# Optimization experiments

Hardware: AMD Instinct MI355X
Metric: run time of the kernel (lower is better)

## Reference

```python
import jax, jax.numpy as jnp
import numpy as np

HIDDEN = 1024
NUM_HEADS = 16
HEAD_DIM = HIDDEN // NUM_HEADS  # 64
MLP_HIDDEN = 4096
RMS_EPS = 1e-6


def setup_inputs() -> dict:
    key = jax.random.key(0)
    ks = jax.random.split(key, 4)
    B, L = 2, 2048
    x = jax.random.normal(ks[0], (B, L, HIDDEN), dtype=jnp.float32)
    pe = jax.random.normal(ks[1], (1, 1, L, HEAD_DIM // 2, 2, 2), dtype=jnp.float32)
    W1 = jax.random.normal(ks[2], (HIDDEN, 3 * HIDDEN + MLP_HIDDEN), dtype=jnp.float32) * (HIDDEN ** -0.5)
    b1 = jnp.zeros((3 * HIDDEN + MLP_HIDDEN,), dtype=jnp.float32)
    W2 = jax.random.normal(ks[3], (HIDDEN + MLP_HIDDEN, HIDDEN), dtype=jnp.float32) * ((HIDDEN + MLP_HIDDEN) ** -0.5)
    b2 = jnp.zeros((HIDDEN,), dtype=jnp.float32)
    q_scale = jnp.ones((HEAD_DIM,), dtype=jnp.float32)
    k_scale = jnp.ones((HEAD_DIM,), dtype=jnp.float32)
    return {"x": x, "pe": pe, "W1": W1, "b1": b1, "W2": W2, "b2": b2,
            "q_scale": q_scale, "k_scale": k_scale}


def _rms_norm(t, scale):
    # RMSNorm over last dim (head_dim) with learnable scale (flux QKNorm)
    rrms = jax.lax.rsqrt(jnp.mean(jnp.square(t), axis=-1, keepdims=True) + RMS_EPS)
    return t * rrms * scale


def _apply_rope(xq, xk, pe):
    # pe: [1,1,L,D/2,2,2]; x*: [B,H,L,D]
    def rope(t):
        t_ = t.reshape(*t.shape[:-1], -1, 1, 2)  # [B,H,L,D/2,1,2]
        out = pe[..., 0] * t_[..., 0] + pe[..., 1] * t_[..., 1]  # [B,H,L,D/2,2]
        return out.reshape(*t.shape)
    return rope(xq), rope(xk)


def reference(x, pe, W1, b1, W2, b2, q_scale, k_scale):
    B, L, _ = x.shape
    h = x @ W1 + b1  # [B,L,3H+Mh]
    qkv, mlp = h[..., : 3 * HIDDEN], h[..., 3 * HIDDEN:]
    # 'B L (K H D) -> K B H L D'
    qkv = qkv.reshape(B, L, 3, NUM_HEADS, HEAD_DIM).transpose(2, 0, 3, 1, 4)
    q, k, v = qkv[0], qkv[1], qkv[2]
    q = _rms_norm(q, q_scale)
    k = _rms_norm(k, k_scale)
    q, k = _apply_rope(q, k, pe)
    scale = HEAD_DIM ** -0.5
    scores = jnp.einsum('bhqd,bhkd->bhqk', q, k) * scale
    attn = jnp.einsum('bhqk,bhkd->bhqd', jax.nn.softmax(scores, axis=-1), v)
    attn = attn.transpose(0, 2, 1, 3).reshape(B, L, HIDDEN)  # 'B H L D -> B L (H D)'
    out = jnp.concatenate((attn, jax.nn.gelu(mlp)), axis=2) @ W2 + b2
    return out
```

## Files before the change

### kernel.cpp

```cpp
#include <hip/hip_runtime.h>

typedef __bf16 bf16;
typedef __bf16 bf16x8 __attribute__((ext_vector_type(8)));
typedef float f32x4 __attribute__((ext_vector_type(4)));
typedef float f32x16 __attribute__((ext_vector_type(16)));

#define GLDS16(gp, lp) __builtin_amdgcn_global_load_lds( \
    (__attribute__((address_space(1))) void*)(gp), \
    (__attribute__((address_space(3))) void*)(lp), 16, 0, 0)

__device__ inline float ex2(float x) { return exp2f(x); }


__global__ void f2b_kernel(const float* __restrict__ src, bf16* __restrict__ dst, long n) {
    long i = ((long)blockIdx.x * 256 + threadIdx.x) * 4;
    if (i + 3 < n) {
        float4 v = *(const float4*)&src[i];
        dst[i + 0] = (bf16)v.x;
        dst[i + 1] = (bf16)v.y;
        dst[i + 2] = (bf16)v.z;
        dst[i + 3] = (bf16)v.w;
    }
}

__global__ __launch_bounds__(256) void transpose_f2b(const float* __restrict__ W,
                                                     bf16* __restrict__ WT,
                                                     int K, int N) {
    __shared__ float tile[32][33];
    int tx = threadIdx.x & 31;
    int ty = threadIdx.x >> 5;
    int n0 = blockIdx.x * 32;
    int k0 = blockIdx.y * 32;
#pragma unroll
    for (int i = 0; i < 4; ++i)
        tile[ty + i * 8][tx] = W[(long)(k0 + ty + i * 8) * N + n0 + tx];
    __syncthreads();
#pragma unroll
    for (int i = 0; i < 4; ++i)
        WT[(long)(n0 + ty + i * 8) * K + k0 + tx] = (bf16)tile[tx][ty + i * 8];
}

template <bool OUT_F32>
__global__ __launch_bounds__(256) void gemm_bt(const bf16* __restrict__ A,
                                               const bf16* __restrict__ BT,
                                               const float* __restrict__ bias,
                                               void* __restrict__ C,
                                               int M, int N, int K) {
    __shared__ bf16 Asm[128 * 32];
    __shared__ bf16 Bsm[128 * 32];
    int tid = threadIdx.x;
    int w = tid >> 6, l = tid & 63;
    int wr = w >> 1, wc = w & 1;
    int bm = blockIdx.x * 128;
    int bn = blockIdx.y * 128;

    f32x4 acc[4][4] = {};

    int arow = l >> 2;
    int acol = (l & 3) * 8;
    int fr = l & 15;
    int fk = (l >> 4) * 8;

    int nk = K >> 5;
    for (int kt = 0; kt < nk; ++kt) {
        int k0 = kt * 32;
#pragma unroll
        for (int it = 0; it < 2; ++it) {
            int c = it * 4 + w;
            const bf16* ga = A + (long)(bm + c * 16 + arow) * K + k0 + acol;
            GLDS16(ga, &Asm[c * 512]);
            const bf16* gb = BT + (long)(bn + c * 16 + arow) * K + k0 + acol;
            GLDS16(gb, &Bsm[c * 512]);
        }
        asm volatile("s_waitcnt vmcnt(0)" ::: "memory");
        __syncthreads();

        bf16x8 af[4], bfr[4];
#pragma unroll
        for (int m = 0; m < 4; ++m)
            af[m] = *(const bf16x8*)&Asm[(wr * 64 + m * 16 + fr) * 32 + fk];
#pragma unroll
        for (int n = 0; n < 4; ++n)
            bfr[n] = *(const bf16x8*)&Bsm[(wc * 64 + n * 16 + fr) * 32 + fk];
#pragma unroll
        for (int m = 0; m < 4; ++m)
#pragma unroll
            for (int n = 0; n < 4; ++n)
                acc[m][n] = __builtin_amdgcn_mfma_f32_16x16x32_bf16(af[m], bfr[n], acc[m][n], 0, 0, 0);
        __syncthreads();
    }

    int orow0 = bm + wr * 64;
    int ocol0 = bn + wc * 64;
#pragma unroll
    for (int m = 0; m < 4; ++m) {
        int row = orow0 + m * 16 + (l >> 4) * 4;
#pragma unroll
        for (int n = 0; n < 4; ++n) {
            int col = ocol0 + n * 16 + (l & 15);
            float bv = bias[col];
#pragma unroll
            for (int r = 0; r < 4; ++r) {
                float v = acc[m][n][r] + bv;
                if (OUT_F32)
                    ((float*)C)[(long)(row + r) * N + col] = v;
                else
                    ((bf16*)C)[(long)(row + r) * N + col] = (bf16)v;
            }
        }
    }
}

__global__ __launch_bounds__(256) void gemm_bt_splitk(const bf16* __restrict__ A,
                                                      const bf16* __restrict__ BT,
                                                      float* __restrict__ part,
                                                      int M, int N, int K, int kchunk) {
    __shared__ bf16 Asm[128 * 32];
    __shared__ bf16 Bsm[128 * 32];
    int tid = threadIdx.x;
    int w = tid >> 6, l = tid & 63;
    int wr = w >> 1, wc = w & 1;
    int bm = blockIdx.x * 128;
    int bn = blockIdx.y * 128;
    int kz = blockIdx.z;

    f32x4 acc[4][4] = {};

    int arow = l >> 2;
    int acol = (l & 3) * 8;
    int fr = l & 15;
    int fk = (l >> 4) * 8;

    int nk = kchunk >> 5;
    for (int kt = 0; kt < nk; ++kt) {
        int k0 = kz * kchunk + kt * 32;
#pragma unroll
        for (int it = 0; it < 2; ++it) {
            int c = it * 4 + w;
            const bf16* ga = A + (long)(bm + c * 16 + arow) * K + k0 + acol;
            GLDS16(ga, &Asm[c * 512]);
            const bf16* gb = BT + (long)(bn + c * 16 + arow) * K + k0 + acol;
            GLDS16(gb, &Bsm[c * 512]);
        }
        asm volatile("s_waitcnt vmcnt(0)" ::: "memory");
        __syncthreads();

        bf16x8 af[4], bfr[4];
#pragma unroll
        for (int m = 0; m < 4; ++m)
            af[m] = *(const bf16x8*)&Asm[(wr * 64 + m * 16 + fr) * 32 + fk];
#pragma unroll
        for (int n = 0; n < 4; ++n)
            bfr[n] = *(const bf16x8*)&Bsm[(wc * 64 + n * 16 + fr) * 32 + fk];
#pragma unroll
        for (int m = 0; m < 4; ++m)
#pragma unroll
            for (int n = 0; n < 4; ++n)
                acc[m][n] = __builtin_amdgcn_mfma_f32_16x16x32_bf16(af[m], bfr[n], acc[m][n], 0, 0, 0);
        __syncthreads();
    }

    float* cz = part + (long)kz * M * N;
    int orow0 = bm + wr * 64;
    int ocol0 = bn + wc * 64;
#pragma unroll
    for (int m = 0; m < 4; ++m) {
        int row = orow0 + m * 16 + (l >> 4) * 4;
#pragma unroll
        for (int n = 0; n < 4; ++n) {
            int col = ocol0 + n * 16 + (l & 15);
#pragma unroll
            for (int r = 0; r < 4; ++r)
                cz[(long)(row + r) * N + col] = acc[m][n][r];
        }
    }
}

__global__ __launch_bounds__(256) void reduce4_kernel(const float* __restrict__ part,
                                                      const float* __restrict__ b2,
                                                      float* __restrict__ out) {
    const long stride4 = 4096L * 1024 / 4;
#pragma unroll
    for (int it = 0; it < 2; ++it) {
        long i4 = (long)blockIdx.x * 512 + it * 256 + threadIdx.x;
        float4 s = *(const float4*)&b2[(i4 * 4) & 1023];
        const float4* p = (const float4*)part;
#pragma unroll
        for (int z = 0; z < 4; ++z) {
            float4 v = p[z * stride4 + i4];
            s.x += v.x; s.y += v.y; s.z += v.z; s.w += v.w;
        }
        *(float4*)&out[i4 * 4] = s;
    }
}

__global__ __launch_bounds__(256) void qkv_kernel(const bf16* __restrict__ h,
                                                  const float* __restrict__ pe,
                                                  const float* __restrict__ qsc_,
                                                  const float* __restrict__ ksc_,
                                                  bf16* __restrict__ qo,
                                                  bf16* __restrict__ ko) {
    int t = blockIdx.x;
    int b = t >> 11;
    int lpos = t & 2047;
    int wv = threadIdx.x >> 6;
    int d = threadIdx.x & 63;
    const bf16* hrow = h + (long)t * 7168;
    float pe0 = pe[lpos * 128 + (d >> 1) * 4 + (d & 1) * 2 + 0];
    float pe1 = pe[lpos * 128 + (d >> 1) * 4 + (d & 1) * 2 + 1];
    float qsc = qsc_[d], ksc = ksc_[d];
#pragma unroll 1
    for (int it = 0; it < 4; ++it) {
        int hh = wv * 4 + it;
        float qv = (float)hrow[hh * 64 + d];
        float kv = (float)hrow[1024 + hh * 64 + d];
        float ssq = qv * qv, ssk = kv * kv;
#pragma unroll
        for (int off = 1; off < 64; off <<= 1) {
            ssq += __shfl_xor(ssq, off, 64);
            ssk += __shfl_xor(ssk, off, 64);
        }
        float qn = qv * rsqrtf(ssq * (1.0f / 64.0f) + 1e-6f) * qsc;
        float kn = kv * rsqrtf(ssk * (1.0f / 64.0f) + 1e-6f) * ksc;
        float qe = __shfl(qn, d & 62, 64), qodd = __shfl(qn, d | 1, 64);
        float ke = __shfl(kn, d & 62, 64), kodd = __shfl(kn, d | 1, 64);
        float qr = (pe0 * qe + pe1 * qodd) * 0.18033688011112042f;
        float kr = pe0 * ke + pe1 * kodd;
        long base = ((long)(b * 16 + hh) * 2048 + lpos) * 64 + d;
        qo[base] = (bf16)qr;
        ko[base] = (bf16)kr;
    }
}

__global__ __launch_bounds__(256) void vtrans_kernel(const bf16* __restrict__ h,
                                                     bf16* __restrict__ vT) {
    __shared__ unsigned short tile[64 * 65];
    int bh = blockIdx.x;
    int b = bh >> 4, hh = bh & 15;
    int l0 = blockIdx.y * 64;
    int tid = threadIdx.x;

    int r = tid >> 3, c = tid & 7;
#pragma unroll
    for (int p = 0; p < 2; ++p) {
        int row = r + p * 32;
        const bf16* src = h + (long)(b * 2048 + l0 + row) * 7168 + 2048 + hh * 64 + c * 8;
        bf16x8 v = *(const bf16x8*)src;
        union { bf16x8 v; unsigned short s[8]; } u; u.v = v;
#pragma unroll
        for (int e = 0; e < 8; ++e) tile[row * 65 + c * 8 + e] = u.s[e];
    }
    __syncthreads();

#pragma unroll
    for (int p = 0; p < 2; ++p) {
        int idx = tid + p * 256;
        int d = idx >> 3, kg = idx & 7;
        union { bf16x8 v; unsigned short s[8]; } u;
#pragma unroll
        for (int e = 0; e < 8; ++e) u.s[e] = tile[(kg * 8 + e) * 65 + d];
        *(bf16x8*)&vT[((long)bh * 64 + d) * 2048 + l0 + kg * 8] = u.v;
    }
}

__global__ void gelu_kernel(const bf16* __restrict__ h, bf16* __restrict__ cat) {
    long e = ((long)blockIdx.x * 256 + threadIdx.x) * 8;
    int t = (int)(e >> 12);
    int j = (int)(e & 4095);
    bf16x8 v = *(const bf16x8*)&h[(long)t * 7168 + 3072 + j];
    bf16x8 o;
#pragma unroll
    for (int r = 0; r < 8; ++r) {
        float x = (float)v[r];
        float g = 0.5f * x * (1.0f + tanhf(0.7978845608028654f * (x + 0.044715f * x * x * x)));
        o[r] = (bf16)g;
    }
    *(bf16x8*)&cat[(long)t * 5120 + 1024 + j] = o;
}

__global__ __launch_bounds__(512) void attn_kernel(const bf16* __restrict__ qg,
                                                   const bf16* __restrict__ kg_,
                                                   const bf16* __restrict__ vT,
                                                   bf16* __restrict__ cat) {
    __shared__ __align__(16) char lds[65536];
    char* Kl0 = lds;
    char* Kl1 = lds + 8192;
    char* Vl0 = lds + 16384;
    char* Vl1 = lds + 24576;

    int bidx = blockIdx.x;
    int bh = bidx & 31;
    int qblk = bidx >> 5;
    int b = bh >> 4, hh = bh & 15;
    int tid = threadIdx.x;
    int wv = tid >> 6, l = tid & 63;
    int h = l >> 5, ln = l & 31;
    int sw = (ln & 7) << 4;

    char* Pw = lds + 32768 + wv * 4096;

    const bf16* qbase = qg + ((long)bh * 2048 + qblk * 256 + wv * 32 + ln) * 64 + h * 8;
    bf16x8 qf[4];
#pragma unroll
    for (int ds = 0; ds < 4; ++ds) qf[ds] = *(const bf16x8*)(qbase + ds * 16);

    f32x16 Oa0 = {}, Oa1 = {};
    float m = -1e30f, lsum = 0.0f;

    int kr = tid >> 3, kg = tid & 7;
    int swb = (kg * 16) ^ ((kr & 7) << 4);
    const bf16* gK = kg_ + ((long)bh * 2048 + kr) * 64 + kg * 8;
    const bf16* gV = vT + ((long)bh * 64 + kr) * 2048 + kg * 8;

    bf16x8 rk = *(const bf16x8*)gK;
    bf16x8 rv = *(const bf16x8*)gV;
    *(bf16x8*)(Kl0 + kr * 128 + swb) = rk;
    *(bf16x8*)(Vl0 + kr * 128 + swb) = rv;
    __syncthreads();

    int c = 0;
    for (int t = 0; t < 32; ++t) {
        if (t < 31) {
            rk = *(const bf16x8*)(gK + (long)(t + 1) * 4096);
            rv = *(const bf16x8*)(gV + (t + 1) * 64);
        }
        const char* Kc = c ? Kl1 : Kl0;
        const char* Vc = c ? Vl1 : Vl0;

        f32x16 S0 = {}, S1 = {};
#pragma unroll
        for (int ds = 0; ds < 4; ++ds) {
            bf16x8 kf0 = *(const bf16x8*)(Kc + ln * 128 + ((ds * 32 + h * 16) ^ sw));
            bf16x8 kf1 = *(const bf16x8*)(Kc + (32 + ln) * 128 + ((ds * 32 + h * 16) ^ sw));
            S0 = __builtin_amdgcn_mfma_f32_32x32x16_bf16(kf0, qf[ds], S0, 0, 0, 0);
            S1 = __builtin_amdgcn_mfma_f32_32x32x16_bf16(kf1, qf[ds], S1, 0, 0, 0);
        }

        float tmax = S0[0];
#pragma unroll
        for (int r = 1; r < 16; ++r) tmax = fmaxf(tmax, S0[r]);
#pragma unroll
        for (int r = 0; r < 16; ++r) tmax = fmaxf(tmax, S1[r]);
        tmax = fmaxf(tmax, __shfl_xor(tmax, 32, 64));

        if (!__all(tmax - m <= 8.0f)) {
            float mn = fmaxf(m, tmax);
            float es = ex2(m - mn);
            lsum *= es;
            m = mn;
#pragma unroll
            for (int r = 0; r < 16; ++r) {
                int rowq = (r & 3) + 8 * (r >> 2) + 4 * h;
                float esr = __shfl(es, rowq, 64);
                Oa0[r] *= esr;
                Oa1[r] *= esr;
            }
        }

        float ps = 0.0f;
#pragma unroll
        for (int kvt = 0; kvt < 2; ++kvt) {
            float p[16];
#pragma unroll
            for (int r = 0; r < 16; ++r) {
                float v = ex2((kvt ? S1[r] : S0[r]) - m);
                p[r] = v;
                ps += v;
            }
#pragma unroll
            for (int i = 0; i < 8; ++i) {
                union { bf16 bb[2]; unsigned u; } pr;
                pr.bb[0] = (bf16)p[2 * i];
                pr.bb[1] = (bf16)p[2 * i + 1];
                int kv = ((2 * i) & 3) + 8 * (i >> 1) + 4 * h + 32 * kvt;
                *(unsigned*)(Pw + ln * 128 + ((kv * 2) ^ sw)) = pr.u;
            }
        }
        lsum += ps + __shfl_xor(ps, 32, 64);

        asm volatile("s_waitcnt lgkmcnt(0)" ::: "memory");

        bf16x8 pa[4];
#pragma unroll
        for (int s = 0; s < 4; ++s)
            pa[s] = *(const bf16x8*)(Pw + ln * 128 + ((s * 32 + h * 16) ^ sw));

#pragma unroll
        for (int s = 0; s < 4; ++s) {
            bf16x8 vf0 = *(const bf16x8*)(Vc + ln * 128 + ((s * 32 + h * 16) ^ sw));
            bf16x8 vf1 = *(const bf16x8*)(Vc + (32 + ln) * 128 + ((s * 32 + h * 16) ^ sw));
            Oa0 = __builtin_amdgcn_mfma_f32_32x32x16_bf16(pa[s], vf0, Oa0, 0, 0, 0);
            Oa1 = __builtin_amdgcn_mfma_f32_32x32x16_bf16(pa[s], vf1, Oa1, 0, 0, 0);
        }

        __syncthreads();
        if (t < 31) {
            char* Kn = c ? Kl0 : Kl1;
            char* Vn = c ? Vl0 : Vl1;
            *(bf16x8*)(Kn + kr * 128 + swb) = rk;
            *(bf16x8*)(Vn + kr * 128 + swb) = rv;
        }
        __syncthreads();
        c ^= 1;
    }

#pragma unroll
    for (int r = 0; r < 16; ++r) {
        int rowq = (r & 3) + 8 * (r >> 2) + 4 * h;
        float ls = __shfl(lsum, rowq, 64);
        float inv = 1.0f / ls;
        long trow = (long)b * 2048 + qblk * 256 + wv * 32 + rowq;
        cat[trow * 5120 + hh * 64 + ln] = (bf16)(Oa0[r] * inv);
        cat[trow * 5120 + hh * 64 + 32 + ln] = (bf16)(Oa1[r] * inv);
    }
}


extern "C" void kernel_launch(void* const* d_in, const int* in_sizes, int n_in,
                              void* d_out, int out_size, void* d_ws, size_t ws_size,
                              hipStream_t stream) {
    const float* x  = (const float*)d_in[0];
    const float* pe = (const float*)d_in[1];
    const float* W1 = (const float*)d_in[2];
    const float* b1 = (const float*)d_in[3];
    const float* W2 = (const float*)d_in[4];
    const float* b2 = (const float*)d_in[5];
    const float* qs = (const float*)d_in[6];
    const float* ks = (const float*)d_in[7];
    float* out = (float*)d_out;

    char* ws = (char*)d_ws;
    bf16* xb  = (bf16*)(ws);
    bf16* w1t = (bf16*)(ws + 8388608);
    bf16* w2t = (bf16*)(ws + 23068672);
    bf16* h   = (bf16*)(ws + 33554432);
    bf16* qb  = (bf16*)(ws + 92274688);
    bf16* kb  = (bf16*)(ws + 100663296);
    bf16* vT  = (bf16*)(ws + 109051904);
    bf16* cat = (bf16*)(ws + 117440512);
    float* part = (float*)(ws + 33554432);

    f2b_kernel<<<4096, 256, 0, stream>>>(x, xb, 4194304L);
    transpose_f2b<<<dim3(224, 32), 256, 0, stream>>>(W1, w1t, 1024, 7168);
    transpose_f2b<<<dim3(32, 160), 256, 0, stream>>>(W2, w2t, 5120, 1024);

    gemm_bt<false><<<dim3(32, 56), 256, 0, stream>>>(xb, w1t, b1, h, 4096, 7168, 1024);

    qkv_kernel<<<4096, 256, 0, stream>>>(h, pe, qs, ks, qb, kb);
    vtrans_kernel<<<dim3(32, 32), 256, 0, stream>>>(h, vT);
    gelu_kernel<<<8192, 256, 0, stream>>>(h, cat);

    attn_kernel<<<256, 512, 0, stream>>>(qb, kb, vT, cat);

    gemm_bt_splitk<<<dim3(32, 8, 4), 256, 0, stream>>>(cat, w2t, part, 4096, 1024, 5120, 1280);
    reduce4_kernel<<<2048, 256, 0, stream>>>(part, b2, out);
}
```

Baseline: 298.3 us.

## Replace GEMMs with pipelined 256x256 tile kernel and fuse GELU into epilogue

Both GEMMs now use one templated kernel with 512 threads and 256x256 output tiles. It double-buffers LDS with asynchronous global-to-LDS loads, staggers the A and B prefetches, raises wave priority around the MFMA bursts, and swizzles the block order for the first GEMM. The first GEMM's epilogue applies GELU to the MLP columns and writes them straight into the concatenated buffer, so the separate GELU kernel and its extra pass over memory are gone. The larger tiles raise register and LDS pressure, and the fewer blocks may leave some CUs idle for the second GEMM.

```diff
diff --git a/kernel.cpp b/kernel.cpp
--- a/kernel.cpp
+++ b/kernel.cpp
@@ -8,6 +8,10 @@
 #define GLDS16(gp, lp) __builtin_amdgcn_global_load_lds( \
     (__attribute__((address_space(1))) void*)(gp), \
     (__attribute__((address_space(3))) void*)(lp), 16, 0, 0)
+
+#define BARRIER() asm volatile("s_barrier" ::: "memory")
+#define LGKM0_FENCE() do { asm volatile("s_waitcnt lgkmcnt(0)" ::: "memory"); \
+                           __builtin_amdgcn_sched_barrier(0); } while (0)
 
 __device__ inline float ex2(float x) { return exp2f(x); }
 
@@ -40,138 +44,140 @@
         WT[(long)(n0 + ty + i * 8) * K + k0 + tx] = (bf16)tile[tx][ty + i * 8];
 }
 
-template <bool OUT_F32>
-__global__ __launch_bounds__(256) void gemm_bt(const bf16* __restrict__ A,
-                                               const bf16* __restrict__ BT,
-                                               const float* __restrict__ bias,
-                                               void* __restrict__ C,
-                                               int M, int N, int K) {
-    __shared__ bf16 Asm[128 * 32];
-    __shared__ bf16 Bsm[128 * 32];
+template <int EPI>
+__global__ __launch_bounds__(512, 2) void gemm256(const bf16* __restrict__ A_,
+                                                  const bf16* __restrict__ BT_,
+                                                  const float* __restrict__ bias,
+                                                  void* __restrict__ C0,
+                                                  void* __restrict__ C1,
+                                                  int M, int N, int K, int kch) {
+    __shared__ __align__(16) char ldsb[65536];
+
+    int bx, by, k0base = 0;
+    if (EPI == 0) {
+        int bid = blockIdx.x;
+        int swz = (bid & 7) * 56 + (bid >> 3);
+        bx = swz & 15; by = swz >> 4;
+    } else {
+        bx = blockIdx.x; by = blockIdx.y;
+        k0base = blockIdx.z * kch;
+    }
+    int bm = bx * 256, bn = by * 256;
+    int NT = kch >> 5;
+
     int tid = threadIdx.x;
     int w = tid >> 6, l = tid & 63;
-    int wr = w >> 1, wc = w & 1;
-    int bm = blockIdx.x * 128;
-    int bn = blockIdx.y * 128;
-
-    f32x4 acc[4][4] = {};
-
-    int arow = l >> 2;
-    int acol = (l & 3) * 8;
-    int fr = l & 15;
-    int fk = (l >> 4) * 8;
-
-    int nk = K >> 5;
-    for (int kt = 0; kt < nk; ++kt) {
-        int k0 = kt * 32;
-#pragma unroll
-        for (int it = 0; it < 2; ++it) {
-            int c = it * 4 + w;
-            const bf16* ga = A + (long)(bm + c * 16 + arow) * K + k0 + acol;
-            GLDS16(ga, &Asm[c * 512]);
-            const bf16* gb = BT + (long)(bn + c * 16 + arow) * K + k0 + acol;
-            GLDS16(gb, &Bsm[c * 512]);
-        }
-        asm volatile("s_waitcnt vmcnt(0)" ::: "memory");
-        __syncthreads();
+    int wr = w >> 2, wc = w & 3;
+    int fr = l & 15, g = l >> 4;
+
+    int srow = tid >> 2;
+    int scol = (tid & 3) * 8;
+    const bf16* gA = A_ + (long)(bm + srow) * K + k0base + scol;
+    const bf16* gB = BT_ + (long)(bn + srow) * K + k0base + scol;
+
+    int abase = (wr * 128 + fr) * 64 + g * 16;
+    int bbase = (wc * 64 + fr) * 64 + g * 16;
+
+    f32x4 acc[8][4] = {};
+
+    GLDS16(gA, ldsb + tid * 16);
+    GLDS16(gA + (long)128 * K, ldsb + 8192 + tid * 16);
+    GLDS16(gB, ldsb + 16384 + tid * 16);
+    GLDS16(gB + (long)128 * K, ldsb + 16384 + 8192 + tid * 16);
+    GLDS16(gB + 32, ldsb + 32768 + 16384 + tid * 16);
+    GLDS16(gB + 32 + (long)128 * K, ldsb + 32768 + 16384 + 8192 + tid * 16);
+    asm volatile("s_waitcnt vmcnt(2)" ::: "memory");
+    BARRIER();
+
+    for (int u = 0; u < NT; ++u) {
+        const char* Ab = ldsb + (u & 1) * 32768;
+        const char* Bb = Ab + 16384;
+        int nxt = (~u) & 1;
 
         bf16x8 af[4], bfr[4];
 #pragma unroll
-        for (int m = 0; m < 4; ++m)
-            af[m] = *(const bf16x8*)&Asm[(wr * 64 + m * 16 + fr) * 32 + fk];
+        for (int i = 0; i < 4; ++i)
+            af[i] = *(const bf16x8*)(Ab + abase + i * 1024);
 #pragma unroll
         for (int n = 0; n < 4; ++n)
-            bfr[n] = *(const bf16x8*)&Bsm[(wc * 64 + n * 16 + fr) * 32 + fk];
-#pragma unroll
-        for (int m = 0; m < 4; ++m)
-#pragma unroll
-            for (int n = 0; n < 4; ++n)
-                acc[m][n] = __builtin_amdgcn_mfma_f32_16x16x32_bf16(af[m], bfr[n], acc[m][n], 0, 0, 0);
-        __syncthreads();
-    }
-
-    int orow0 = bm + wr * 64;
-    int ocol0 = bn + wc * 64;
-#pragma unroll
-    for (int m = 0; m < 4; ++m) {
-        int row = orow0 + m * 16 + (l >> 4) * 4;
-#pragma unroll
-        for (int n = 0; n < 4; ++n) {
-            int col = ocol0 + n * 16 + (l & 15);
-            float bv = bias[col];
-#pragma unroll
-            for (int r = 0; r < 4; ++r) {
-                float v = acc[m][n][r] + bv;
-                if (OUT_F32)
-                    ((float*)C)[(long)(row + r) * N + col] = v;
-                else
-                    ((bf16*)C)[(long)(row + r) * N + col] = (bf16)v;
+            bfr[n] = *(const bf16x8*)(Bb + bbase + n * 1024);
+        if (u + 1 < NT) {
+            const bf16* s = gA + (u + 1) * 32;
+            GLDS16(s, ldsb + nxt * 32768 + tid * 16);
+            GLDS16(s + (long)128 * K, ldsb + nxt * 32768 + 8192 + tid * 16);
+        }
+        BARRIER();
+        LGKM0_FENCE();
+        __builtin_amdgcn_s_setprio(1);
+#pragma unroll
+        for (int n = 0; n < 4; ++n)
+#pragma unroll
+            for (int i = 0; i < 4; ++i)
+                acc[i][n] = __builtin_amdgcn_mfma_f32_16x16x32_bf16(af[i], bfr[n], acc[i][n], 0, 0, 0);
+        __builtin_amdgcn_s_setprio(0);
+        BARRIER();
+
+#pragma unroll
+        for (int i = 0; i < 4; ++i)
+            af[i] = *(const bf16x8*)(Ab + abase + (4 + i) * 1024);
+        if (u + 2 < NT) {
+            const bf16* s = gB + (u + 2) * 32;
+            GLDS16(s, ldsb + (u & 1) * 32768 + 16384 + tid * 16);
+            GLDS16(s + (long)128 * K, ldsb + (u & 1) * 32768 + 16384 + 8192 + tid * 16);
+        }
+        BARRIER();
+        LGKM0_FENCE();
+        __builtin_amdgcn_s_setprio(1);
+#pragma unroll
+        for (int n = 0; n < 4; ++n)
+#pragma unroll
+            for (int i = 0; i < 4; ++i)
+                acc[4 + i][n] = __builtin_amdgcn_mfma_f32_16x16x32_bf16(af[i], bfr[n], acc[4 + i][n], 0, 0, 0);
+        __builtin_amdgcn_s_setprio(0);
+        if (u < NT - 2) {
+            asm volatile("s_waitcnt vmcnt(2)" ::: "memory");
+        } else {
+            asm volatile("s_waitcnt vmcnt(0)" ::: "memory");
+        }
+        BARRIER();
+    }
+
+    int r4 = (l >> 4) * 4;
+    if (EPI == 0) {
+        bf16* hp = (bf16*)C0;
+        bf16* cat = (bf16*)C1;
+        bool gel = (bn >= 3072);
+#pragma unroll
+        for (int mi = 0; mi < 8; ++mi) {
+            int row = bm + wr * 128 + mi * 16 + r4;
+#pragma unroll
+            for (int n = 0; n < 4; ++n) {
+                int col = bn + wc * 64 + n * 16 + fr;
+                float bv = bias[col];
+#pragma unroll
+                for (int r = 0; r < 4; ++r) {
+                    float v = acc[mi][n][r] + bv;
+                    if (gel) {
+                        float gg = 0.5f * v * (1.0f + tanhf(0.7978845608028654f * (v + 0.044715f * v * v * v)));
+                        cat[(long)(row + r) * 5120 + 1024 + col - 3072] = (bf16)gg;
+                    } else {
+                        hp[(long)(row + r) * N + col] = (bf16)v;
+                    }
+                }
             }
         }
-    }
-}
-
-__global__ __launch_bounds__(256) void gemm_bt_splitk(const bf16* __restrict__ A,
-                                                      const bf16* __restrict__ BT,
-                                                      float* __restrict__ part,
-                                                      int M, int N, int K, int kchunk) {
-    __shared__ bf16 Asm[128 * 32];
-    __shared__ bf16 Bsm[128 * 32];
-    int tid = threadIdx.x;
-    int w = tid >> 6, l = tid & 63;
-    int wr = w >> 1, wc = w & 1;
-    int bm = blockIdx.x * 128;
-    int bn = blockIdx.y * 128;
-    int kz = blockIdx.z;
-
-    f32x4 acc[4][4] = {};
-
-    int arow = l >> 2;
-    int acol = (l & 3) * 8;
-    int fr = l & 15;
-    int fk = (l >> 4) * 8;
-
-    int nk = kchunk >> 5;
-    for (int kt = 0; kt < nk; ++kt) {
-        int k0 = kz * kchunk + kt * 32;
-#pragma unroll
-        for (int it = 0; it < 2; ++it) {
-            int c = it * 4 + w;
-            const bf16* ga = A + (long)(bm + c * 16 + arow) * K + k0 + acol;
-            GLDS16(ga, &Asm[c * 512]);
-            const bf16* gb = BT + (long)(bn + c * 16 + arow) * K + k0 + acol;
-            GLDS16(gb, &Bsm[c * 512]);
-        }
-        asm volatile("s_waitcnt vmcnt(0)" ::: "memory");
-        __syncthreads();
-
-        bf16x8 af[4], bfr[4];
-#pragma unroll
-        for (int m = 0; m < 4; ++m)
-            af[m] = *(const bf16x8*)&Asm[(wr * 64 + m * 16 + fr) * 32 + fk];
-#pragma unroll
-        for (int n = 0; n < 4; ++n)
-            bfr[n] = *(const bf16x8*)&Bsm[(wc * 64 + n * 16 + fr) * 32 + fk];
-#pragma unroll
-        for (int m = 0; m < 4; ++m)
-#pragma unroll
-            for (int n = 0; n < 4; ++n)
-                acc[m][n] = __builtin_amdgcn_mfma_f32_16x16x32_bf16(af[m], bfr[n], acc[m][n], 0, 0, 0);
-        __syncthreads();
-    }
-
-    float* cz = part + (long)kz * M * N;
-    int orow0 = bm + wr * 64;
-    int ocol0 = bn + wc * 64;
-#pragma unroll
-    for (int m = 0; m < 4; ++m) {
-        int row = orow0 + m * 16 + (l >> 4) * 4;
-#pragma unroll
-        for (int n = 0; n < 4; ++n) {
-            int col = ocol0 + n * 16 + (l & 15);
-#pragma unroll
-            for (int r = 0; r < 4; ++r)
-                cz[(long)(row + r) * N + col] = acc[m][n][r];
+    } else {
+        float* cz = (float*)C0 + (long)blockIdx.z * M * N;
+#pragma unroll
+        for (int mi = 0; mi < 8; ++mi) {
+            int row = bm + wr * 128 + mi * 16 + r4;
+#pragma unroll
+            for (int n = 0; n < 4; ++n) {
+                int col = bn + wc * 64 + n * 16 + fr;
+#pragma unroll
+                for (int r = 0; r < 4; ++r)
+                    cz[(long)(row + r) * N + col] = acc[mi][n][r];
+            }
         }
     }
 }
@@ -251,7 +257,6 @@
         for (int e = 0; e < 8; ++e) tile[row * 65 + c * 8 + e] = u.s[e];
     }
     __syncthreads();
-
 #pragma unroll
     for (int p = 0; p < 2; ++p) {
         int idx = tid + p * 256;
@@ -261,21 +266,6 @@
         for (int e = 0; e < 8; ++e) u.s[e] = tile[(kg * 8 + e) * 65 + d];
         *(bf16x8*)&vT[((long)bh * 64 + d) * 2048 + l0 + kg * 8] = u.v;
     }
-}
-
-__global__ void gelu_kernel(const bf16* __restrict__ h, bf16* __restrict__ cat) {
-    long e = ((long)blockIdx.x * 256 + threadIdx.x) * 8;
-    int t = (int)(e >> 12);
-    int j = (int)(e & 4095);
-    bf16x8 v = *(const bf16x8*)&h[(long)t * 7168 + 3072 + j];
-    bf16x8 o;
-#pragma unroll
-    for (int r = 0; r < 8; ++r) {
-        float x = (float)v[r];
-        float g = 0.5f * x * (1.0f + tanhf(0.7978845608028654f * (x + 0.044715f * x * x * x)));
-        o[r] = (bf16)g;
-    }
-    *(bf16x8*)&cat[(long)t * 5120 + 1024 + j] = o;
 }
 
 __global__ __launch_bounds__(512) void attn_kernel(const bf16* __restrict__ qg,
@@ -444,14 +434,13 @@
     transpose_f2b<<<dim3(224, 32), 256, 0, stream>>>(W1, w1t, 1024, 7168);
     transpose_f2b<<<dim3(32, 160), 256, 0, stream>>>(W2, w2t, 5120, 1024);
 
-    gemm_bt<false><<<dim3(32, 56), 256, 0, stream>>>(xb, w1t, b1, h, 4096, 7168, 1024);
+    gemm256<0><<<dim3(448), 512, 0, stream>>>(xb, w1t, b1, h, cat, 4096, 7168, 1024, 1024);
 
     qkv_kernel<<<4096, 256, 0, stream>>>(h, pe, qs, ks, qb, kb);
     vtrans_kernel<<<dim3(32, 32), 256, 0, stream>>>(h, vT);
-    gelu_kernel<<<8192, 256, 0, stream>>>(h, cat);
 
     attn_kernel<<<256, 512, 0, stream>>>(qb, kb, vT, cat);
 
-    gemm_bt_splitk<<<dim3(32, 8, 4), 256, 0, stream>>>(cat, w2t, part, 4096, 1024, 5120, 1280);
+    gemm256<1><<<dim3(16, 4, 4), 512, 0, stream>>>(cat, w2t, nullptr, part, nullptr, 4096, 1024, 5120, 1280);
     reduce4_kernel<<<2048, 256, 0, stream>>>(part, b2, out);
 }
```

Result: faster. 290.5 us (-2.6%).

## Fuse GELU into first GEMM epilogue and pipeline attention K/V with async LDS loads

Applied to the files above, without the earlier changes.

The first GEMM epilogue now applies tanh-GELU to the MLP columns and writes them straight into the concat buffer. This removes the separate gelu kernel, along with its read of the MLP half of h and the GEMM's write of it. The attention kernel moves to 256-thread blocks covering 128 queries each, with twice as many blocks. It streams K/V through a triple-buffered LDS ring using global_load_lds with partial vmcnt waits, one barrier per tile, and s_setprio around the MFMA sections. The split-K GEMM is merged into the templated GEMM. The risks are a heavier GEMM epilogue (tanhf per element on a subset of blocks) and more LDS traffic per query from reloading K/V across twice as many blocks.

```diff
diff --git a/kernel.cpp b/kernel.cpp
--- a/kernel.cpp
+++ b/kernel.cpp
@@ -8,6 +8,8 @@
 #define GLDS16(gp, lp) __builtin_amdgcn_global_load_lds( \
     (__attribute__((address_space(1))) void*)(gp), \
     (__attribute__((address_space(3))) void*)(lp), 16, 0, 0)
+
+#define BARRIER() asm volatile("s_barrier" ::: "memory")
 
 __device__ inline float ex2(float x) { return exp2f(x); }
 
@@ -40,12 +42,13 @@
         WT[(long)(n0 + ty + i * 8) * K + k0 + tx] = (bf16)tile[tx][ty + i * 8];
 }
 
-template <bool OUT_F32>
+template <int EPI>
 __global__ __launch_bounds__(256) void gemm_bt(const bf16* __restrict__ A,
                                                const bf16* __restrict__ BT,
                                                const float* __restrict__ bias,
-                                               void* __restrict__ C,
-                                               int M, int N, int K) {
+                                               void* __restrict__ C0,
+                                               void* __restrict__ C1,
+                                               int M, int N, int K, int kch) {
     __shared__ bf16 Asm[128 * 32];
     __shared__ bf16 Bsm[128 * 32];
     int tid = threadIdx.x;
@@ -53,6 +56,7 @@
     int wr = w >> 1, wc = w & 1;
     int bm = blockIdx.x * 128;
     int bn = blockIdx.y * 128;
+    int k0base = (EPI == 1) ? blockIdx.z * kch : 0;
 
     f32x4 acc[4][4] = {};
 
@@ -61,9 +65,9 @@
     int fr = l & 15;
     int fk = (l >> 4) * 8;
 
-    int nk = K >> 5;
+    int nk = kch >> 5;
     for (int kt = 0; kt < nk; ++kt) {
-        int k0 = kt * 32;
+        int k0 = k0base + kt * 32;
 #pragma unroll
         for (int it = 0; it < 2; ++it) {
             int c = it * 4 + w;
@@ -92,86 +96,41 @@
 
     int orow0 = bm + wr * 64;
     int ocol0 = bn + wc * 64;
-#pragma unroll
-    for (int m = 0; m < 4; ++m) {
-        int row = orow0 + m * 16 + (l >> 4) * 4;
-#pragma unroll
-        for (int n = 0; n < 4; ++n) {
-            int col = ocol0 + n * 16 + (l & 15);
-            float bv = bias[col];
-#pragma unroll
-            for (int r = 0; r < 4; ++r) {
-                float v = acc[m][n][r] + bv;
-                if (OUT_F32)
-                    ((float*)C)[(long)(row + r) * N + col] = v;
-                else
-                    ((bf16*)C)[(long)(row + r) * N + col] = (bf16)v;
-            }
-        }
-    }
-}
-
-__global__ __launch_bounds__(256) void gemm_bt_splitk(const bf16* __restrict__ A,
-                                                      const bf16* __restrict__ BT,
-                                                      float* __restrict__ part,
-                                                      int M, int N, int K, int kchunk) {
-    __shared__ bf16 Asm[128 * 32];
-    __shared__ bf16 Bsm[128 * 32];
-    int tid = threadIdx.x;
-    int w = tid >> 6, l = tid & 63;
-    int wr = w >> 1, wc = w & 1;
-    int bm = blockIdx.x * 128;
-    int bn = blockIdx.y * 128;
-    int kz = blockIdx.z;
-
-    f32x4 acc[4][4] = {};
-
-    int arow = l >> 2;
-    int acol = (l & 3) * 8;
-    int fr = l & 15;
-    int fk = (l >> 4) * 8;
-
-    int nk = kchunk >> 5;
-    for (int kt = 0; kt < nk; ++kt) {
-        int k0 = kz * kchunk + kt * 32;
-#pragma unroll
-        for (int it = 0; it < 2; ++it) {
-            int c = it * 4 + w;
-            const bf16* ga = A + (long)(bm + c * 16 + arow) * K + k0 + acol;
-            GLDS16(ga, &Asm[c * 512]);
-            const bf16* gb = BT + (long)(bn + c * 16 + arow) * K + k0 + acol;
-            GLDS16(gb, &Bsm[c * 512]);
-        }
-        asm volatile("s_waitcnt vmcnt(0)" ::: "memory");
-        __syncthreads();
-
-        bf16x8 af[4], bfr[4];
-#pragma unroll
-        for (int m = 0; m < 4; ++m)
-            af[m] = *(const bf16x8*)&Asm[(wr * 64 + m * 16 + fr) * 32 + fk];
-#pragma unroll
-        for (int n = 0; n < 4; ++n)
-            bfr[n] = *(const bf16x8*)&Bsm[(wc * 64 + n * 16 + fr) * 32 + fk];
-#pragma unroll
-        for (int m = 0; m < 4; ++m)
-#pragma unroll
-            for (int n = 0; n < 4; ++n)
-                acc[m][n] = __builtin_amdgcn_mfma_f32_16x16x32_bf16(af[m], bfr[n], acc[m][n], 0, 0, 0);
-        __syncthreads();
-    }
-
-    float* cz = part + (long)kz * M * N;
-    int orow0 = bm + wr * 64;
-    int ocol0 = bn + wc * 64;
-#pragma unroll
-    for (int m = 0; m < 4; ++m) {
-        int row = orow0 + m * 16 + (l >> 4) * 4;
-#pragma unroll
-        for (int n = 0; n < 4; ++n) {
-            int col = ocol0 + n * 16 + (l & 15);
-#pragma unroll
-            for (int r = 0; r < 4; ++r)
-                cz[(long)(row + r) * N + col] = acc[m][n][r];
+    if (EPI == 0) {
+        bf16* hp = (bf16*)C0;
+        bf16* cat = (bf16*)C1;
+        bool gel = (bn >= 3072);
+#pragma unroll
+        for (int m = 0; m < 4; ++m) {
+            int row = orow0 + m * 16 + (l >> 4) * 4;
+#pragma unroll
+            for (int n = 0; n < 4; ++n) {
+                int col = ocol0 + n * 16 + (l & 15);
+                float bv = bias[col];
+#pragma unroll
+                for (int r = 0; r < 4; ++r) {
+                    float v = acc[m][n][r] + bv;
+                    if (gel) {
+                        float gg = 0.5f * v * (1.0f + tanhf(0.7978845608028654f * (v + 0.044715f * v * v * v)));
+                        cat[(long)(row + r) * 5120 + 1024 + col - 3072] = (bf16)gg;
+                    } else {
+                        hp[(long)(row + r) * N + col] = (bf16)v;
+                    }
+                }
+            }
+        }
+    } else {
+        float* cz = (float*)C0 + (long)blockIdx.z * M * N;
+#pragma unroll
+        for (int m = 0; m < 4; ++m) {
+            int row = orow0 + m * 16 + (l >> 4) * 4;
+#pragma unroll
+            for (int n = 0; n < 4; ++n) {
+                int col = ocol0 + n * 16 + (l & 15);
+#pragma unroll
+                for (int r = 0; r < 4; ++r)
+                    cz[(long)(row + r) * N + col] = acc[m][n][r];
+            }
         }
     }
 }
@@ -251,7 +210,6 @@
         for (int e = 0; e < 8; ++e) tile[row * 65 + c * 8 + e] = u.s[e];
     }
     __syncthreads();
-
 #pragma unroll
     for (int p = 0; p < 2; ++p) {
         int idx = tid + p * 256;
@@ -263,43 +221,23 @@
     }
 }
 
-__global__ void gelu_kernel(const bf16* __restrict__ h, bf16* __restrict__ cat) {
-    long e = ((long)blockIdx.x * 256 + threadIdx.x) * 8;
-    int t = (int)(e >> 12);
-    int j = (int)(e & 4095);
-    bf16x8 v = *(const bf16x8*)&h[(long)t * 7168 + 3072 + j];
-    bf16x8 o;
-#pragma unroll
-    for (int r = 0; r < 8; ++r) {
-        float x = (float)v[r];
-        float g = 0.5f * x * (1.0f + tanhf(0.7978845608028654f * (x + 0.044715f * x * x * x)));
-        o[r] = (bf16)g;
-    }
-    *(bf16x8*)&cat[(long)t * 5120 + 1024 + j] = o;
-}
-
-__global__ __launch_bounds__(512) void attn_kernel(const bf16* __restrict__ qg,
+__global__ __launch_bounds__(256) void attn_kernel(const bf16* __restrict__ qg,
                                                    const bf16* __restrict__ kg_,
                                                    const bf16* __restrict__ vT,
                                                    bf16* __restrict__ cat) {
     __shared__ __align__(16) char lds[65536];
-    char* Kl0 = lds;
-    char* Kl1 = lds + 8192;
-    char* Vl0 = lds + 16384;
-    char* Vl1 = lds + 24576;
-
-    int bidx = blockIdx.x;
-    int bh = bidx & 31;
-    int qblk = bidx >> 5;
+
+    int bh = blockIdx.x & 31;
+    int qblk = blockIdx.x >> 5;
     int b = bh >> 4, hh = bh & 15;
     int tid = threadIdx.x;
     int wv = tid >> 6, l = tid & 63;
     int h = l >> 5, ln = l & 31;
     int sw = (ln & 7) << 4;
 
-    char* Pw = lds + 32768 + wv * 4096;
-
-    const bf16* qbase = qg + ((long)bh * 2048 + qblk * 256 + wv * 32 + ln) * 64 + h * 8;
+    char* Pw = lds + 49152 + wv * 4096;
+
+    const bf16* qbase = qg + ((long)bh * 2048 + qblk * 128 + wv * 32 + ln) * 64 + h * 8;
     bf16x8 qf[4];
 #pragma unroll
     for (int ds = 0; ds < 4; ++ds) qf[ds] = *(const bf16x8*)(qbase + ds * 16);
@@ -307,27 +245,34 @@
     f32x16 Oa0 = {}, Oa1 = {};
     float m = -1e30f, lsum = 0.0f;
 
-    int kr = tid >> 3, kg = tid & 7;
-    int swb = (kg * 16) ^ ((kr & 7) << 4);
-    const bf16* gK = kg_ + ((long)bh * 2048 + kr) * 64 + kg * 8;
-    const bf16* gV = vT + ((long)bh * 64 + kr) * 2048 + kg * 8;
-
-    bf16x8 rk = *(const bf16x8*)gK;
-    bf16x8 rv = *(const bf16x8*)gV;
-    *(bf16x8*)(Kl0 + kr * 128 + swb) = rk;
-    *(bf16x8*)(Vl0 + kr * 128 + swb) = rv;
-    __syncthreads();
-
-    int c = 0;
+    int srow = tid >> 3;
+    int sgran = (tid & 7) ^ (srow & 7);
+    const bf16* gK = kg_ + ((long)bh * 2048 + srow) * 64 + sgran * 8;
+    const bf16* gV = vT + ((long)bh * 64 + srow) * 2048 + sgran * 8;
+
+    GLDS16(gK, lds + tid * 16);
+    GLDS16(gK + 2048, lds + 4096 + tid * 16);
+    GLDS16(gV, lds + 24576 + tid * 16);
+    GLDS16(gV + 32 * 2048, lds + 24576 + 4096 + tid * 16);
+
+    int bi = 0, bn_ = 1;
     for (int t = 0; t < 32; ++t) {
-        if (t < 31) {
-            rk = *(const bf16x8*)(gK + (long)(t + 1) * 4096);
-            rv = *(const bf16x8*)(gV + (t + 1) * 64);
-        }
-        const char* Kc = c ? Kl1 : Kl0;
-        const char* Vc = c ? Vl1 : Vl0;
+        if (t + 1 < 32) {
+            GLDS16(gK + (long)(t + 1) * 4096, lds + bn_ * 8192 + tid * 16);
+            GLDS16(gK + (long)(t + 1) * 4096 + 2048, lds + bn_ * 8192 + 4096 + tid * 16);
+            GLDS16(gV + (t + 1) * 64, lds + 24576 + bn_ * 8192 + tid * 16);
+            GLDS16(gV + (t + 1) * 64 + 32 * 2048, lds + 24576 + bn_ * 8192 + 4096 + tid * 16);
+            asm volatile("s_waitcnt vmcnt(4)" ::: "memory");
+        } else {
+            asm volatile("s_waitcnt vmcnt(0)" ::: "memory");
+        }
+        BARRIER();
+
+        const char* Kc = lds + bi * 8192;
+        const char* Vc = lds + 24576 + bi * 8192;
 
         f32x16 S0 = {}, S1 = {};
+        __builtin_amdgcn_s_setprio(1);
 #pragma unroll
         for (int ds = 0; ds < 4; ++ds) {
             bf16x8 kf0 = *(const bf16x8*)(Kc + ln * 128 + ((ds * 32 + h * 16) ^ sw));
@@ -335,6 +280,7 @@
             S0 = __builtin_amdgcn_mfma_f32_32x32x16_bf16(kf0, qf[ds], S0, 0, 0, 0);
             S1 = __builtin_amdgcn_mfma_f32_32x32x16_bf16(kf1, qf[ds], S1, 0, 0, 0);
         }
+        __builtin_amdgcn_s_setprio(0);
 
         float tmax = S0[0];
 #pragma unroll
@@ -385,6 +331,7 @@
         for (int s = 0; s < 4; ++s)
             pa[s] = *(const bf16x8*)(Pw + ln * 128 + ((s * 32 + h * 16) ^ sw));
 
+        __builtin_amdgcn_s_setprio(1);
 #pragma unroll
         for (int s = 0; s < 4; ++s) {
             bf16x8 vf0 = *(const bf16x8*)(Vc + ln * 128 + ((s * 32 + h * 16) ^ sw));
@@ -392,16 +339,10 @@
             Oa0 = __builtin_amdgcn_mfma_f32_32x32x16_bf16(pa[s], vf0, Oa0, 0, 0, 0);
             Oa1 = __builtin_amdgcn_mfma_f32_32x32x16_bf16(pa[s], vf1, Oa1, 0, 0, 0);
         }
-
-        __syncthreads();
-        if (t < 31) {
-            char* Kn = c ? Kl0 : Kl1;
-            char* Vn = c ? Vl0 : Vl1;
-            *(bf16x8*)(Kn + kr * 128 + swb) = rk;
-            *(bf16x8*)(Vn + kr * 128 + swb) = rv;
-        }
-        __syncthreads();
-        c ^= 1;
+        __builtin_amdgcn_s_setprio(0);
+
+        bi = bn_;
+        bn_ = (bn_ == 2) ? 0 : bn_ + 1;
     }
 
 #pragma unroll
@@ -409,7 +350,7 @@
         int rowq = (r & 3) + 8 * (r >> 2) + 4 * h;
         float ls = __shfl(lsum, rowq, 64);
         float inv = 1.0f / ls;
-        long trow = (long)b * 2048 + qblk * 256 + wv * 32 + rowq;
+        long trow = (long)b * 2048 + qblk * 128 + wv * 32 + rowq;
         cat[trow * 5120 + hh * 64 + ln] = (bf16)(Oa0[r] * inv);
         cat[trow * 5120 + hh * 64 + 32 + ln] = (bf16)(Oa1[r] * inv);
     }
@@ -444,14 +385,13 @@
     transpose_f2b<<<dim3(224, 32), 256, 0, stream>>>(W1, w1t, 1024, 7168);
     transpose_f2b<<<dim3(32, 160), 256, 0, stream>>>(W2, w2t, 5120, 1024);
 
-    gemm_bt<false><<<dim3(32, 56), 256, 0, stream>>>(xb, w1t, b1, h, 4096, 7168, 1024);
+    gemm_bt<0><<<dim3(32, 56), 256, 0, stream>>>(xb, w1t, b1, h, cat, 4096, 7168, 1024, 1024);
 
     qkv_kernel<<<4096, 256, 0, stream>>>(h, pe, qs, ks, qb, kb);
     vtrans_kernel<<<dim3(32, 32), 256, 0, stream>>>(h, vT);
-    gelu_kernel<<<8192, 256, 0, stream>>>(h, cat);
-
-    attn_kernel<<<256, 512, 0, stream>>>(qb, kb, vT, cat);
-
-    gemm_bt_splitk<<<dim3(32, 8, 4), 256, 0, stream>>>(cat, w2t, part, 4096, 1024, 5120, 1280);
+
+    attn_kernel<<<512, 256, 0, stream>>>(qb, kb, vT, cat);
+
+    gemm_bt<1><<<dim3(32, 8, 4), 256, 0, stream>>>(cat, w2t, nullptr, part, nullptr, 4096, 1024, 5120, 1280);
     reduce4_kernel<<<2048, 256, 0, stream>>>(part, b2, out);
 }
```

Result: no change. 302.8 us (+1.5%).
